# Optimization experiments

Measured on AMD Instinct MI355X. Metric: run time of the kernel, lower is better.

Reference implementation:

```python
import jax, jax.numpy as jnp
import numpy as np

DIM = 128
N = 2048
M = 2048


def setup_inputs() -> dict:
    key = jax.random.key(0)
    k1, k2, k3, k4, k5, k6 = jax.random.split(key, 6)
    s1 = 1.0 / np.sqrt(2 * DIM)  # torch Linear default init bound
    s2 = 1.0 / np.sqrt(DIM)
    return {
        "z_i": jax.random.normal(k1, (N, DIM), dtype=jnp.float32),
        "z_j": jax.random.normal(k2, (M, DIM), dtype=jnp.float32),
        "W1": jax.random.uniform(k3, (2 * DIM, DIM), minval=-s1, maxval=s1, dtype=jnp.float32),
        "b1": jax.random.uniform(k4, (DIM,), minval=-s1, maxval=s1, dtype=jnp.float32),
        "W2": jax.random.uniform(k5, (DIM, 1), minval=-s2, maxval=s2, dtype=jnp.float32),
        "b2": jax.random.uniform(k6, (1,), minval=-s2, maxval=s2, dtype=jnp.float32),
    }


def reference(z_i, z_j, W1, b1, W2, b2):
    # Linear(cat([zi, zj])) == zi @ W1[:dim] + zj @ W1[dim:] + b1 -- same math
    # as the torch module, without materializing the [N, M, 2*dim] concat.
    hi = z_i @ W1[:DIM]  # [N, dim]
    hj = z_j @ W1[DIM:]  # [M, dim]
    h = jax.nn.relu(hi[:, None, :] + hj[None, :, :] + b1)  # [N, M, dim]
    out = h @ W2 + b2  # [N, M, 1]
    return out[..., 0]  # [N, M]
```

## Files before the change

### kernel.cpp

```cpp
#include <hip/hip_runtime.h>

#define DIM 128
#define NROWS 2048
#define NDP 64

typedef float v2f __attribute__((ext_vector_type(2)));
typedef _Float16 h2 __attribute__((ext_vector_type(2)));

static __device__ __forceinline__ h2 u2h(unsigned u) { return __builtin_bit_cast(h2, u); }
static __device__ __forceinline__ unsigned h2u(h2 h) { return __builtin_bit_cast(unsigned, h); }

__global__ __launch_bounds__(512) void prep_kernel(
    const float* __restrict__ z_i, const float* __restrict__ z_j,
    const float* __restrict__ W1, const float* __restrict__ b1,
    unsigned* __restrict__ hi2T, unsigned* __restrict__ hj2T) {
  __shared__ float wlds[DIM * DIM];

  const int t = threadIdx.x;
  const int side = blockIdx.y;
  const int rowbase = blockIdx.x * 8;
  const float* w = W1 + side * (DIM * DIM);

#pragma unroll
  for (int rep = 0; rep < 8; ++rep) {
    const int idx = rep * 512 + t;
    *(float4*)(wlds + idx * 4) = *(const float4*)(w + idx * 4);
  }
  __syncthreads();

  const int row = rowbase + (t >> 6);
  const int dp = t & 63;
  const float* zrow = (side ? z_j : z_i) + (size_t)row * DIM;

  v2f acc = {0.f, 0.f};
#pragma unroll 8
  for (int k = 0; k < DIM; ++k) {
    const float zv = zrow[k];
    const v2f wv = *(const v2f*)(wlds + k * DIM + dp * 2);
    acc = __builtin_elementwise_fma(wv, (v2f){zv, zv}, acc);
  }

  if (side) {
    acc.x += b1[2 * dp];
    acc.y += b1[2 * dp + 1];
  }
  h2 hv = {(_Float16)acc.x, (_Float16)acc.y};
  unsigned* dst = side ? hj2T : hi2T;
  dst[(size_t)dp * NROWS + row] = h2u(hv);
}

__global__ __launch_bounds__(256) void score_kernel(
    const unsigned* __restrict__ hi2T, const unsigned* __restrict__ hj2T,
    const float* __restrict__ W2, const float* __restrict__ b2p,
    float* __restrict__ out) {
  __shared__ unsigned his2[NDP * 64];
  __shared__ unsigned hjs2[NDP * 128];
  __shared__ unsigned w2s[NDP];

  const int t = threadIdx.x;
  const int ibase = blockIdx.y * 64;
  const int jbase = blockIdx.x * 128;

#pragma unroll
  for (int rep = 0; rep < 4; ++rep) {
    const int idx = rep * 256 + t;
    const int dp = idx >> 4, c = (idx & 15) * 4;
    *(uint4*)(his2 + dp * 64 + c) =
        *(const uint4*)(hi2T + (size_t)dp * NROWS + ibase + c);
  }
#pragma unroll
  for (int rep = 0; rep < 8; ++rep) {
    const int idx = rep * 256 + t;
    const int dp = idx >> 5, c = (idx & 31) * 4;
    *(uint4*)(hjs2 + dp * 128 + c) =
        *(const uint4*)(hj2T + (size_t)dp * NROWS + jbase + c);
  }
  if (t < NDP) {
    h2 wp = {(_Float16)W2[2 * t], (_Float16)W2[2 * t + 1]};
    w2s[t] = h2u(wp);
  }
  __syncthreads();

  const int tx = t & 15;
  const int ty = t >> 4;

  float acc[4][8];
#pragma unroll
  for (int ii = 0; ii < 4; ++ii)
#pragma unroll
    for (int jj = 0; jj < 8; ++jj) acc[ii][jj] = 0.f;

#pragma unroll 8
  for (int dp = 0; dp < NDP; ++dp) {
    const uint4 hu = *(const uint4*)(his2 + dp * 64 + ty * 4);
    const uint4 ju0 = *(const uint4*)(hjs2 + dp * 128 + tx * 8);
    const uint4 ju1 = *(const uint4*)(hjs2 + dp * 128 + tx * 8 + 4);
    const h2 wp = u2h(w2s[dp]);
    const h2 hiv[4] = {u2h(hu.x), u2h(hu.y), u2h(hu.z), u2h(hu.w)};
    const h2 hjv[8] = {u2h(ju0.x), u2h(ju0.y), u2h(ju0.z), u2h(ju0.w),
                       u2h(ju1.x), u2h(ju1.y), u2h(ju1.z), u2h(ju1.w)};
    const h2 zero = {(_Float16)0.f, (_Float16)0.f};
#pragma unroll
    for (int ii = 0; ii < 4; ++ii) {
#pragma unroll
      for (int jj = 0; jj < 8; ++jj) {
        h2 s = hiv[ii] + hjv[jj];
        s = __builtin_elementwise_max(s, zero);
        acc[ii][jj] = __builtin_amdgcn_fdot2(s, wp, acc[ii][jj], false);
      }
    }
  }

  const float bias = *b2p;
#pragma unroll
  for (int ii = 0; ii < 4; ++ii) {
    const int i = ibase + ty * 4 + ii;
    float* o = out + (size_t)i * NROWS + jbase + tx * 8;
    const float4 o0 = {acc[ii][0] + bias, acc[ii][1] + bias,
                       acc[ii][2] + bias, acc[ii][3] + bias};
    const float4 o1 = {acc[ii][4] + bias, acc[ii][5] + bias,
                       acc[ii][6] + bias, acc[ii][7] + bias};
    *(float4*)o = o0;
    *(float4*)(o + 4) = o1;
  }
}

extern "C" void kernel_launch(void* const* d_in, const int* in_sizes, int n_in,
                              void* d_out, int out_size, void* d_ws, size_t ws_size,
                              hipStream_t stream) {
  const float* z_i = (const float*)d_in[0];
  const float* z_j = (const float*)d_in[1];
  const float* W1  = (const float*)d_in[2];
  const float* b1  = (const float*)d_in[3];
  const float* W2  = (const float*)d_in[4];
  const float* b2  = (const float*)d_in[5];
  float* out = (float*)d_out;

  unsigned* hi2T = (unsigned*)d_ws;
  unsigned* hj2T = hi2T + (size_t)NDP * NROWS;

  prep_kernel<<<dim3(256, 2), 512, 0, stream>>>(z_i, z_j, W1, b1, hi2T, hj2T);
  score_kernel<<<dim3(16, 32), 256, 0, stream>>>(hi2T, hj2T, W2, b2, out);
}
```

Baseline: 106.2 us.

## Shrink score tile to 64x64 and restructure prep to stage z in LDS

The prep kernel no longer copies the 64KB W1 slice into LDS. It stages the 8 z rows in LDS, reads W1 columns from global memory, and has each thread compute two rows, which cuts LDS footprint and the per-block W1 load. The score kernel drops from a 64x128 tile to 64x64 with 4x4 outputs per thread and twice as many blocks, and it declares an occupancy hint and loads W2 pairs once per group of four dp. This trades less data reuse per block for more blocks and lower register and LDS pressure in exchange for better occupancy.

```diff
diff --git a/kernel.cpp b/kernel.cpp
--- a/kernel.cpp
+++ b/kernel.cpp
@@ -10,56 +10,57 @@
 static __device__ __forceinline__ h2 u2h(unsigned u) { return __builtin_bit_cast(h2, u); }
 static __device__ __forceinline__ unsigned h2u(h2 h) { return __builtin_bit_cast(unsigned, h); }
 
-__global__ __launch_bounds__(512) void prep_kernel(
+__global__ __launch_bounds__(256) void prep_kernel(
     const float* __restrict__ z_i, const float* __restrict__ z_j,
     const float* __restrict__ W1, const float* __restrict__ b1,
     unsigned* __restrict__ hi2T, unsigned* __restrict__ hj2T) {
-  __shared__ float wlds[DIM * DIM];
+  __shared__ float zs[8 * DIM];
 
   const int t = threadIdx.x;
   const int side = blockIdx.y;
   const int rowbase = blockIdx.x * 8;
-  const float* w = W1 + side * (DIM * DIM);
 
-#pragma unroll
-  for (int rep = 0; rep < 8; ++rep) {
-    const int idx = rep * 512 + t;
-    *(float4*)(wlds + idx * 4) = *(const float4*)(w + idx * 4);
-  }
+  const float* z = (side ? z_j : z_i) + (size_t)rowbase * DIM;
+  ((float4*)zs)[t] = ((const float4*)z)[t];
   __syncthreads();
 
-  const int row = rowbase + (t >> 6);
   const int dp = t & 63;
-  const float* zrow = (side ? z_j : z_i) + (size_t)row * DIM;
+  const int rg = t >> 6;
+  const float* wcol = W1 + side * (DIM * DIM) + dp * 2;
+  const float* z0 = zs + (rg * 2) * DIM;
+  const float* z1 = z0 + DIM;
 
-  v2f acc = {0.f, 0.f};
+  v2f acc0 = {0.f, 0.f}, acc1 = {0.f, 0.f};
 #pragma unroll 8
   for (int k = 0; k < DIM; ++k) {
-    const float zv = zrow[k];
-    const v2f wv = *(const v2f*)(wlds + k * DIM + dp * 2);
-    acc = __builtin_elementwise_fma(wv, (v2f){zv, zv}, acc);
+    const v2f wv = *(const v2f*)(wcol + (size_t)k * DIM);
+    const float a = z0[k], b = z1[k];
+    acc0 = __builtin_elementwise_fma(wv, (v2f){a, a}, acc0);
+    acc1 = __builtin_elementwise_fma(wv, (v2f){b, b}, acc1);
   }
 
   if (side) {
-    acc.x += b1[2 * dp];
-    acc.y += b1[2 * dp + 1];
+    const v2f bb = *(const v2f*)(b1 + dp * 2);
+    acc0 += bb;
+    acc1 += bb;
   }
-  h2 hv = {(_Float16)acc.x, (_Float16)acc.y};
-  unsigned* dst = side ? hj2T : hi2T;
-  dst[(size_t)dp * NROWS + row] = h2u(hv);
+  unsigned* dst = (side ? hj2T : hi2T) + (size_t)dp * NROWS + rowbase + rg * 2;
+  dst[0] = h2u((h2){(_Float16)acc0.x, (_Float16)acc0.y});
+  dst[1] = h2u((h2){(_Float16)acc1.x, (_Float16)acc1.y});
 }
 
-__global__ __launch_bounds__(256) void score_kernel(
+__global__ __launch_bounds__(256, 4) void score_kernel(
     const unsigned* __restrict__ hi2T, const unsigned* __restrict__ hj2T,
     const float* __restrict__ W2, const float* __restrict__ b2p,
     float* __restrict__ out) {
   __shared__ unsigned his2[NDP * 64];
-  __shared__ unsigned hjs2[NDP * 128];
+  __shared__ unsigned hjs2[NDP * 64];
   __shared__ unsigned w2s[NDP];
 
   const int t = threadIdx.x;
   const int ibase = blockIdx.y * 64;
-  const int jbase = blockIdx.x * 128;
+  const int jbase = blockIdx.x * 64;
+  const float bias = *b2p;
 
 #pragma unroll
   for (int rep = 0; rep < 4; ++rep) {
@@ -67,61 +68,55 @@
     const int dp = idx >> 4, c = (idx & 15) * 4;
     *(uint4*)(his2 + dp * 64 + c) =
         *(const uint4*)(hi2T + (size_t)dp * NROWS + ibase + c);
-  }
-#pragma unroll
-  for (int rep = 0; rep < 8; ++rep) {
-    const int idx = rep * 256 + t;
-    const int dp = idx >> 5, c = (idx & 31) * 4;
-    *(uint4*)(hjs2 + dp * 128 + c) =
+    *(uint4*)(hjs2 + dp * 64 + c) =
         *(const uint4*)(hj2T + (size_t)dp * NROWS + jbase + c);
   }
   if (t < NDP) {
-    h2 wp = {(_Float16)W2[2 * t], (_Float16)W2[2 * t + 1]};
-    w2s[t] = h2u(wp);
+    const v2f wp = *(const v2f*)(W2 + t * 2);
+    w2s[t] = h2u((h2){(_Float16)wp.x, (_Float16)wp.y});
   }
   __syncthreads();
 
   const int tx = t & 15;
   const int ty = t >> 4;
 
-  float acc[4][8];
+  float acc[4][4];
 #pragma unroll
   for (int ii = 0; ii < 4; ++ii)
 #pragma unroll
-    for (int jj = 0; jj < 8; ++jj) acc[ii][jj] = 0.f;
+    for (int jj = 0; jj < 4; ++jj) acc[ii][jj] = 0.f;
 
-#pragma unroll 8
-  for (int dp = 0; dp < NDP; ++dp) {
-    const uint4 hu = *(const uint4*)(his2 + dp * 64 + ty * 4);
-    const uint4 ju0 = *(const uint4*)(hjs2 + dp * 128 + tx * 8);
-    const uint4 ju1 = *(const uint4*)(hjs2 + dp * 128 + tx * 8 + 4);
-    const h2 wp = u2h(w2s[dp]);
-    const h2 hiv[4] = {u2h(hu.x), u2h(hu.y), u2h(hu.z), u2h(hu.w)};
-    const h2 hjv[8] = {u2h(ju0.x), u2h(ju0.y), u2h(ju0.z), u2h(ju0.w),
-                       u2h(ju1.x), u2h(ju1.y), u2h(ju1.z), u2h(ju1.w)};
-    const h2 zero = {(_Float16)0.f, (_Float16)0.f};
+  const h2 zero = {(_Float16)0.f, (_Float16)0.f};
+#pragma unroll 2
+  for (int dpg = 0; dpg < 16; ++dpg) {
+    const uint4 w4 = *(const uint4*)(w2s + dpg * 4);
+    const h2 wp[4] = {u2h(w4.x), u2h(w4.y), u2h(w4.z), u2h(w4.w)};
 #pragma unroll
-    for (int ii = 0; ii < 4; ++ii) {
+    for (int q = 0; q < 4; ++q) {
+      const int dp = dpg * 4 + q;
+      const uint4 hu = *(const uint4*)(his2 + dp * 64 + ty * 4);
+      const uint4 ju = *(const uint4*)(hjs2 + dp * 64 + tx * 4);
+      const h2 hiv[4] = {u2h(hu.x), u2h(hu.y), u2h(hu.z), u2h(hu.w)};
+      const h2 hjv[4] = {u2h(ju.x), u2h(ju.y), u2h(ju.z), u2h(ju.w)};
 #pragma unroll
-      for (int jj = 0; jj < 8; ++jj) {
-        h2 s = hiv[ii] + hjv[jj];
-        s = __builtin_elementwise_max(s, zero);
-        acc[ii][jj] = __builtin_amdgcn_fdot2(s, wp, acc[ii][jj], false);
+      for (int ii = 0; ii < 4; ++ii) {
+#pragma unroll
+        for (int jj = 0; jj < 4; ++jj) {
+          h2 s = hiv[ii] + hjv[jj];
+          s = __builtin_elementwise_max(s, zero);
+          acc[ii][jj] = __builtin_amdgcn_fdot2(s, wp[q], acc[ii][jj], false);
+        }
       }
     }
   }
 
-  const float bias = *b2p;
 #pragma unroll
   for (int ii = 0; ii < 4; ++ii) {
     const int i = ibase + ty * 4 + ii;
-    float* o = out + (size_t)i * NROWS + jbase + tx * 8;
-    const float4 o0 = {acc[ii][0] + bias, acc[ii][1] + bias,
+    float* o = out + (size_t)i * NROWS + jbase + tx * 4;
+    const float4 ov = {acc[ii][0] + bias, acc[ii][1] + bias,
                        acc[ii][2] + bias, acc[ii][3] + bias};
-    const float4 o1 = {acc[ii][4] + bias, acc[ii][5] + bias,
-                       acc[ii][6] + bias, acc[ii][7] + bias};
-    *(float4*)o = o0;
-    *(float4*)(o + 4) = o1;
+    *(float4*)o = ov;
   }
 }
 
@@ -139,6 +134,6 @@
   unsigned* hi2T = (unsigned*)d_ws;
   unsigned* hj2T = hi2T + (size_t)NDP * NROWS;
 
-  prep_kernel<<<dim3(256, 2), 512, 0, stream>>>(z_i, z_j, W1, b1, hi2T, hj2T);
-  score_kernel<<<dim3(16, 32), 256, 0, stream>>>(hi2T, hj2T, W2, b2, out);
+  prep_kernel<<<dim3(256, 2), 256, 0, stream>>>(z_i, z_j, W1, b1, hi2T, hj2T);
+  score_kernel<<<dim3(32, 32), 256, 0, stream>>>(hi2T, hj2T, W2, b2, out);
 }
```

New measurement: 105.3 us. No clear change (-0.9%).
